# Optimization experiments

Measured on AMD Instinct MI355X. Metric: run time of the kernel, lower is better.

The kernel has to match this reference:

```python
import jax, jax.numpy as jnp
import numpy as np

N, L, D = 8192, 50, 64          # nodes, max history length, embed_dim
NUM_USERS = 100000
NUM_ITEMS = 100000
NUM_RATINGS = 5


def setup_inputs() -> dict:
    key = jax.random.key(0)
    ks = jax.random.split(key, 12)
    g = lambda k, shp, s=0.05: jax.random.normal(k, shp, jnp.float32) * s
    return {
        "nodes": jax.random.randint(ks[0], (N,), 0, NUM_USERS),
        "history_uv": jax.random.randint(ks[1], (N, L), 0, NUM_ITEMS),
        "history_r": jax.random.randint(ks[2], (N, L), 0, NUM_RATINGS),
        "hist_len": jax.random.randint(ks[3], (N,), 1, L + 1),  # ragged lengths in [1, L]
        # embedding tables (v2e / u2e / r2e)
        "v2e": g(ks[4], (NUM_ITEMS, D), 0.1),
        "u2e": g(ks[5], (NUM_USERS, D), 0.1),
        "r2e": g(ks[6], (NUM_RATINGS, D), 0.1),
        # w_r1: Dense(2D -> D), w_r2: Dense(D -> D)
        "W1": g(ks[7], (2 * D, D)), "b1": jnp.zeros((D,), jnp.float32),
        "W2": g(ks[8], (D, D)), "b2": jnp.zeros((D,), jnp.float32),
        # Attention MLP: Dense(2D->D), Dense(D->D), Dense(D->1)
        "A1": g(ks[9], (2 * D, D)), "ab1": jnp.zeros((D,), jnp.float32),
        "A2": g(ks[10], (D, D)), "ab2": jnp.zeros((D,), jnp.float32),
        "A3": g(ks[11], (D, 1)), "ab3": jnp.zeros((1,), jnp.float32),
    }


def reference(nodes, history_uv, history_r, hist_len, v2e, u2e, r2e,
              W1, b1, W2, b2, A1, ab1, A2, ab2, A3, ab3):
    # Vectorized form of the per-node Python loop: pad histories to L, mask.
    e_uv = v2e[history_uv]                       # [N,L,D] neighbor item embeds
    uv_rep = u2e[nodes]                          # [N,D]   self (user) embed
    e_r = r2e[history_r]                         # [N,L,D] rating embeds
    x = jnp.concatenate([e_uv, e_r], axis=-1)    # [N,L,2D]
    x = jax.nn.relu(x @ W1 + b1)                 # w_r1 + relu
    o = jax.nn.relu(x @ W2 + b2)                 # w_r2 + relu -> o_history [N,L,D]
    # attention: concat(o_history, repeated uv_rep) -> 2-layer relu MLP -> scalar
    a_in = jnp.concatenate(
        [o, jnp.broadcast_to(uv_rep[:, None, :], o.shape)], axis=-1)  # [N,L,2D]
    h = jax.nn.relu(a_in @ A1 + ab1)
    h = jax.nn.relu(h @ A2 + ab2)
    s = (h @ A3 + ab3)[..., 0]                   # [N,L] attention logits
    mask = jnp.arange(L)[None, :] < hist_len[:, None]
    att = jax.nn.softmax(jnp.where(mask, s, -1e9), axis=-1)  # softmax over history
    # att_history = o_history^T @ att_w, per node -> [N,D]
    return jnp.einsum('nl,nld->nd', att, o)
```

## Files before the change

### kernel.cpp

```cpp
#include <hip/hip_runtime.h>
#include <hip/hip_bf16.h>
#include <stdint.h>

typedef short bfx8 __attribute__((ext_vector_type(8)));
typedef float f32x4 __attribute__((ext_vector_type(4)));

#define MFMA16(a, b, c) __builtin_amdgcn_mfma_f32_16x16x32_bf16(a, b, c, 0, 0, 0)
#define STAGE_FENCE() __builtin_amdgcn_sched_barrier(0x77)
#define PIN_FENCE()   __builtin_amdgcn_sched_barrier(0x47)

#define OFF_W1 0
#define OFF_A1 8192
#define OFF_W2 24576
#define OFF_A2 32768
#define OFF_CB 40960
#define OFF_TB 42256
#define CBB_B1  0
#define CBB_B2  256
#define CBB_AB1 512
#define CBB_AB2 768
#define CBB_A3  1024

__device__ __forceinline__ uint32_t pk2(float a, float b) {
    __hip_bfloat162 h = __float22bfloat162_rn(make_float2(a, b));
    union { __hip_bfloat162 h; uint32_t u; } cv; cv.h = h; return cv.u;
}
__device__ __forceinline__ float bflo(uint32_t w) { return __uint_as_float(w << 16); }
__device__ __forceinline__ float bfhi(uint32_t w) { return __uint_as_float(w & 0xFFFF0000u); }

__device__ __forceinline__ bfx8 pack8(const float4 a, const float4 b) {
    union { bfx8 v; uint32_t u[4]; } r;
    r.u[0] = pk2(a.x, a.y); r.u[1] = pk2(a.z, a.w);
    r.u[2] = pk2(b.x, b.y); r.u[3] = pk2(b.z, b.w);
    return r.v;
}
__device__ __forceinline__ bfx8 packr(f32x4 a, f32x4 b) {
    union { bfx8 v; uint32_t u[4]; } r;
    r.u[0] = pk2(fmaxf(a[0], 0.f), fmaxf(a[1], 0.f));
    r.u[1] = pk2(fmaxf(a[2], 0.f), fmaxf(a[3], 0.f));
    r.u[2] = pk2(fmaxf(b[0], 0.f), fmaxf(b[1], 0.f));
    r.u[3] = pk2(fmaxf(b[2], 0.f), fmaxf(b[3], 0.f));
    return r.v;
}
__device__ __forceinline__ float4 ld4(const float* p) { return *(const float4*)p; }

__device__ __forceinline__ int mix4(int row) {
    return (row & 3) | (((row >> 4) & 1) << 2) | (((row >> 3) & 1) << 3);
}
__device__ __forceinline__ int mix3(int row) {
    return (row & 3) | (((row >> 3) & 1) << 2);
}
template <int CTRL>
__device__ __forceinline__ float dppadd(float x) {
    int y = __builtin_amdgcn_update_dpp(0, __float_as_int(x), CTRL, 0xF, 0xF, false);
    return x + __int_as_float(y);
}
__device__ __forceinline__ float rowsum16(float x) {
    x = dppadd<0xB1>(x);
    x = dppadd<0x4E>(x);
    x = dppadd<0x124>(x);
    x = dppadd<0x128>(x);
    return x;
}

__global__ __launch_bounds__(512, 1) void uvagg_mfma(
    const int* __restrict__ nodes, const int* __restrict__ huv,
    const int* __restrict__ hr, const int* __restrict__ hlen,
    const float* __restrict__ v2e, const float* __restrict__ u2e,
    const float* __restrict__ r2e,
    const float* __restrict__ W1, const float* __restrict__ b1,
    const float* __restrict__ W2, const float* __restrict__ b2,
    const float* __restrict__ A1, const float* __restrict__ ab1,
    const float* __restrict__ A2, const float* __restrict__ ab2,
    const float* __restrict__ A3, const float* __restrict__ ab3f,
    float* __restrict__ out, int N, int L, int nwaves)
{
    __shared__ __align__(16) uint8_t smem[43616];
    float* cbf = (float*)(smem + OFF_CB);

    const int tid = threadIdx.x;
    for (int i = tid; i < 4096; i += 512) {
        int kp = i >> 6, d = i & 63;
        int addr = d * 256 + ((((kp >> 2) ^ mix4(d)) & 15) << 4) + ((kp & 3) << 2);
        *(uint32_t*)(smem + OFF_A1 + addr) = pk2(A1[(2 * kp) * 64 + d], A1[(2 * kp + 1) * 64 + d]);
    }
    for (int i = tid; i < 2048; i += 512) {
        int kp = i >> 6, d = i & 63;
        int addr = d * 128 + ((((kp >> 2) ^ mix3(d)) & 7) << 4) + ((kp & 3) << 2);
        *(uint32_t*)(smem + OFF_W1 + addr) = pk2(W1[(2 * kp) * 64 + d], W1[(2 * kp + 1) * 64 + d]);
        *(uint32_t*)(smem + OFF_W2 + addr) = pk2(W2[(2 * kp) * 64 + d], W2[(2 * kp + 1) * 64 + d]);
        *(uint32_t*)(smem + OFF_A2 + addr) = pk2(A2[(2 * kp) * 64 + d], A2[(2 * kp + 1) * 64 + d]);
    }
    for (int i = tid; i < 321; i += 512) {
        if (i < 64)       cbf[i]   = b1[i];
        else if (i < 128) cbf[i]   = b2[i - 64];
        else if (i < 192) cbf[i]   = ab1[i - 128];
        else if (i < 256) cbf[i]   = ab2[i - 192];
        else if (i < 320) cbf[i]   = A3[i - 256];
        else              cbf[320] = ab3f[0];
    }
    for (int i = tid; i < 320; i += 512) {
        const int rr_ = i >> 6, d = i & 63;
        const float* wcol = W1 + 64 * 64 + d;
        const float* rrow = r2e + rr_ * 64;
        float a0 = b1[d], a1 = 0.f, a2 = 0.f, a3 = 0.f;
        #pragma unroll
        for (int k2 = 0; k2 < 64; k2 += 4) {
            a0 = fmaf(wcol[(k2 + 0) * 64], rrow[k2 + 0], a0);
            a1 = fmaf(wcol[(k2 + 1) * 64], rrow[k2 + 1], a1);
            a2 = fmaf(wcol[(k2 + 2) * 64], rrow[k2 + 2], a2);
            a3 = fmaf(wcol[(k2 + 3) * 64], rrow[k2 + 3], a3);
        }
        *(float*)(smem + OFF_TB + rr_ * 272 + d * 4) = (a0 + a1) + (a2 + a3);
    }
    __syncthreads();

    const int lane = tid & 63;
    const int wid  = tid >> 6;
    const int s    = lane & 15;
    const int g    = lane >> 4;
    const int r    = s & 3;
    const int q    = s >> 2;
    const int rs   = 8 * q + r;

    const int cx = ((q >> 1) | ((q & 1) << 1));
    const int base1 = rs * 256 + ((g ^ r) << 4) + (cx << 6);
    const int base2 = rs * 128 + ((g ^ r) << 4) + ((q & 1) << 6);
    const uint8_t* pw2 = smem + (base1 ^ (2 << 6));
    const uint8_t* pw3 = smem + (base1 ^ (3 << 6));
    const uint8_t* pa0 = smem + (base1 ^ (0 << 6));
    const uint8_t* pa1 = smem + (base1 ^ (1 << 6));
    const uint8_t* pq0 = smem + (base2 ^ (0 << 6));
    const uint8_t* pq1 = smem + (base2 ^ (1 << 6));
    const uint8_t* pcb = smem + OFF_CB + 32 * g;
    const uint8_t* ptb = smem + OFF_TB + 32 * g;
    const float ab3 = cbf[320];

    for (int node = blockIdx.x * 8 + wid; node < N; node += nwaves) {
        const int hl = __builtin_amdgcn_readfirstlane(min(hlen[node], L));
        const int un = __builtin_amdgcn_readfirstlane(nodes[node]);

        const float* ur = u2e + (size_t)un * 64;
        const bfx8 uf2 = pack8(ld4(ur + 8 * g),      ld4(ur + 8 * g + 4));
        const bfx8 uf3 = pack8(ld4(ur + 32 + 8 * g), ld4(ur + 36 + 8 * g));

        const int idxlane = min(lane, L - 1);
        const int iu_all = huv[(size_t)node * L + idxlane];
        const int ir_all = hr [(size_t)node * L + idxlane];

        f32x4 h1base[4];
        #pragma unroll
        for (int mt = 0; mt < 4; ++mt) {
            const int dof = 4 * (mt & 1) + 32 * (mt >> 1);
            h1base[mt] = *(const f32x4*)(pcb + CBB_AB1 + dof * 4);
            h1base[mt] = MFMA16(*(const bfx8*)(pw2 + OFF_A1 + dof * 256), uf2, h1base[mt]);
            h1base[mt] = MFMA16(*(const bfx8*)(pw3 + OFF_A1 + dof * 256), uf3, h1base[mt]);
        }

        float zacc = 0.0f;
        f32x4 accO[4];
        #pragma unroll
        for (int i = 0; i < 4; ++i) accO[i] = f32x4{0.f, 0.f, 0.f, 0.f};

        const int ntile = (hl + 15) >> 4;

        float4 qa0, qa1, qa2, qa3;
        int irs;
        {
            const int slot0 = min(s, hl - 1);
            const int iu = __shfl(iu_all, slot0, 64);
            irs = __shfl(ir_all, slot0, 64);
            const float* vr = v2e + (size_t)iu * 64;
            qa0 = ld4(vr + 8 * g);      qa1 = ld4(vr + 8 * g + 4);
            qa2 = ld4(vr + 32 + 8 * g); qa3 = ld4(vr + 36 + 8 * g);
        }

        for (int tt = 0; tt < ntile; ++tt) {
            const int gslot = tt * 16 + s;
            const bfx8 f0 = pack8(qa0, qa1);
            const bfx8 f1 = pack8(qa2, qa3);
            const uint8_t* ptbr = ptb + irs * 272;

            f32x4 ah[4];
            #pragma unroll
            for (int mt = 0; mt < 4; ++mt) {
                const int dof = 4 * (mt & 1) + 32 * (mt >> 1);
                ah[mt] = *(const f32x4*)(ptbr + dof * 4);
                ah[mt] = MFMA16(*(const bfx8*)(pq0 + OFF_W1 + dof * 128), f0, ah[mt]);
                ah[mt] = MFMA16(*(const bfx8*)(pq1 + OFF_W1 + dof * 128), f1, ah[mt]);
            }
            const bfx8 x1a = packr(ah[0], ah[1]);
            const bfx8 x1b = packr(ah[2], ah[3]);

            if (tt + 1 < ntile) {
                const int nslot = min(tt * 16 + 16 + s, hl - 1);
                const int niu = __shfl(iu_all, nslot, 64);
                irs = __shfl(ir_all, nslot, 64);
                const float* vr = v2e + (size_t)niu * 64;
                qa0 = ld4(vr + 8 * g);      qa1 = ld4(vr + 8 * g + 4);
                qa2 = ld4(vr + 32 + 8 * g); qa3 = ld4(vr + 36 + 8 * g);
            }
            PIN_FENCE();

            f32x4 ao[4];
            #pragma unroll
            for (int mt = 0; mt < 4; ++mt) {
                const int dof = 4 * (mt & 1) + 32 * (mt >> 1);
                ao[mt] = *(const f32x4*)(pcb + CBB_B2 + dof * 4);
                ao[mt] = MFMA16(*(const bfx8*)(pq0 + OFF_W2 + dof * 128), x1a, ao[mt]);
                ao[mt] = MFMA16(*(const bfx8*)(pq1 + OFF_W2 + dof * 128), x1b, ao[mt]);
            }
            const bfx8 oa = packr(ao[0], ao[1]);
            const bfx8 ob = packr(ao[2], ao[3]);
            STAGE_FENCE();

            f32x4 h[4];
            #pragma unroll
            for (int mt = 0; mt < 4; ++mt) {
                const int dof = 4 * (mt & 1) + 32 * (mt >> 1);
                h[mt] = h1base[mt];
                h[mt] = MFMA16(*(const bfx8*)(pa0 + OFF_A1 + dof * 256), oa, h[mt]);
                h[mt] = MFMA16(*(const bfx8*)(pa1 + OFF_A1 + dof * 256), ob, h[mt]);
            }
            const bfx8 h1a = packr(h[0], h[1]);
            const bfx8 h1b = packr(h[2], h[3]);
            STAGE_FENCE();

            float part = 0.0f;
            #pragma unroll
            for (int mt = 0; mt < 4; ++mt) {
                const int dof = 4 * (mt & 1) + 32 * (mt >> 1);
                f32x4 h2 = *(const f32x4*)(pcb + CBB_AB2 + dof * 4);
                h2 = MFMA16(*(const bfx8*)(pq0 + OFF_A2 + dof * 128), h1a, h2);
                h2 = MFMA16(*(const bfx8*)(pq1 + OFF_A2 + dof * 128), h1b, h2);
                const f32x4 aq = *(const f32x4*)(pcb + CBB_A3 + dof * 4);
                part = fmaf(fmaxf(h2[0], 0.f), aq[0], part);
                part = fmaf(fmaxf(h2[1], 0.f), aq[1], part);
                part = fmaf(fmaxf(h2[2], 0.f), aq[2], part);
                part = fmaf(fmaxf(h2[3], 0.f), aq[3], part);
            }
            STAGE_FENCE();
            float p2 = part + __shfl_xor(part, 16, 64);
            const float sl = p2 + __shfl_xor(p2, 32, 64) + ab3;
            const float p = (gslot < hl) ? __expf(sl) : 0.0f;
            zacc += p;
            union { bfx8 v; uint32_t u[4]; } ua, ub;
            ua.v = oa; ub.v = ob;
            #pragma unroll
            for (int j = 0; j < 2; ++j) {
                accO[0][2*j+0] = fmaf(p, bflo(ua.u[j]),     accO[0][2*j+0]);
                accO[0][2*j+1] = fmaf(p, bfhi(ua.u[j]),     accO[0][2*j+1]);
                accO[1][2*j+0] = fmaf(p, bflo(ua.u[2 + j]), accO[1][2*j+0]);
                accO[1][2*j+1] = fmaf(p, bfhi(ua.u[2 + j]), accO[1][2*j+1]);
                accO[2][2*j+0] = fmaf(p, bflo(ub.u[j]),     accO[2][2*j+0]);
                accO[2][2*j+1] = fmaf(p, bfhi(ub.u[j]),     accO[2][2*j+1]);
                accO[3][2*j+0] = fmaf(p, bflo(ub.u[2 + j]), accO[3][2*j+0]);
                accO[3][2*j+1] = fmaf(p, bfhi(ub.u[2 + j]), accO[3][2*j+1]);
            }
        }

        const float Z = rowsum16(zacc);
        #pragma unroll
        for (int mt = 0; mt < 4; ++mt)
            #pragma unroll
            for (int rr2 = 0; rr2 < 4; ++rr2)
                accO[mt][rr2] = rowsum16(accO[mt][rr2]);
        const float inv = 1.0f / Z;
        if (s == 0) {
            float* op = out + (size_t)node * 64;
            #pragma unroll
            for (int mt = 0; mt < 4; ++mt) {
                const int dof = 8 * g + 4 * (mt & 1) + 32 * (mt >> 1);
                *(float4*)(op + dof) = make_float4(accO[mt][0] * inv, accO[mt][1] * inv,
                                                   accO[mt][2] * inv, accO[mt][3] * inv);
            }
        }
    }
}

extern "C" void kernel_launch(void* const* d_in, const int* in_sizes, int n_in,
                              void* d_out, int out_size, void* d_ws, size_t ws_size,
                              hipStream_t stream) {
    const int*   nodes = (const int*)d_in[0];
    const int*   huv   = (const int*)d_in[1];
    const int*   hrr   = (const int*)d_in[2];
    const int*   hlen  = (const int*)d_in[3];
    const float* v2e   = (const float*)d_in[4];
    const float* u2e   = (const float*)d_in[5];
    const float* r2e   = (const float*)d_in[6];
    const float* W1    = (const float*)d_in[7];
    const float* b1    = (const float*)d_in[8];
    const float* W2    = (const float*)d_in[9];
    const float* b2    = (const float*)d_in[10];
    const float* A1    = (const float*)d_in[11];
    const float* ab1   = (const float*)d_in[12];
    const float* A2    = (const float*)d_in[13];
    const float* ab2   = (const float*)d_in[14];
    const float* A3    = (const float*)d_in[15];
    const float* ab3   = (const float*)d_in[16];
    float* out = (float*)d_out;

    const int N = in_sizes[0];
    const int L = in_sizes[1] / N;

    int blocks = (N + 7) / 8;
    if (blocks > 768) blocks = 768;
    const int nwaves = blocks * 8;

    hipLaunchKernelGGL(uvagg_mfma, dim3(blocks), dim3(512), 0, stream,
                       nodes, huv, hrr, hlen, v2e, u2e, r2e,
                       W1, b1, W2, b2, A1, ab1, A2, ab2, A3, ab3,
                       out, N, L, nwaves);
}
```

Measured before the change: 41.51 us.

## Sort nodes by history-length bin and pair long/short nodes per wave

Adds three small pre-kernels that bucket nodes by tile count (ceil(hist_len/16)), prefix-scan the per-wave bin counts, and scatter node indices into a sorted permutation. The main kernel then gives each wave a pair of nodes taken from opposite ends of the sorted order, so every wave gets a roughly equal amount of work. The grid is also reduced to 512 blocks. This targets the tail imbalance caused by ragged history lengths, at the cost of three extra kernel launches and an indirect node lookup.

New measurement: 47.34 us. +14.0%, slower.

```diff
diff --git a/kernel.cpp b/kernel.cpp
--- a/kernel.cpp
+++ b/kernel.cpp
@@ -63,6 +63,54 @@
     return x;
 }
 
+__global__ __launch_bounds__(256) void bin_count(const int* __restrict__ hlen,
+                                                 int N, int L, int* __restrict__ wavecnt) {
+    const int i = blockIdx.x * 256 + threadIdx.x;
+    const int ww = i >> 6, lane = i & 63;
+    const int NW = (N + 63) >> 6;
+    int bin = -1;
+    if (i < N) bin = ((min(hlen[i], L) + 15) >> 4) - 1;
+    #pragma unroll
+    for (int b = 0; b < 4; ++b) {
+        unsigned long long m = __ballot(bin == b);
+        if (lane == 0 && ww < NW) wavecnt[b * NW + ww] = __popcll(m);
+    }
+}
+
+__global__ __launch_bounds__(512) void bin_scan(int* __restrict__ wavecnt, int n) {
+    __shared__ int sa[512], sb[512];
+    const int t = threadIdx.x;
+    const int v = (t < n) ? wavecnt[t] : 0;
+    sa[t] = v;
+    __syncthreads();
+    int* src = sa; int* dst = sb;
+    #pragma unroll
+    for (int off = 1; off < 512; off <<= 1) {
+        dst[t] = src[t] + ((t >= off) ? src[t - off] : 0);
+        __syncthreads();
+        int* tmp = src; src = dst; dst = tmp;
+    }
+    if (t < n) wavecnt[t] = src[t] - v;
+}
+
+__global__ __launch_bounds__(256) void bin_scatter(const int* __restrict__ hlen,
+                                                   int N, int L,
+                                                   const int* __restrict__ offs,
+                                                   int* __restrict__ perm) {
+    const int i = blockIdx.x * 256 + threadIdx.x;
+    const int ww = i >> 6, lane = i & 63;
+    const int NW = (N + 63) >> 6;
+    const int bin = (i < N) ? (((min(hlen[i], L) + 15) >> 4) - 1) : -1;
+    #pragma unroll
+    for (int b = 0; b < 4; ++b) {
+        unsigned long long m = __ballot(bin == b);
+        if (bin == b) {
+            int rank = __popcll(m & ((1ULL << lane) - 1ULL));
+            perm[offs[b * NW + ww] + rank] = i;
+        }
+    }
+}
+
 __global__ __launch_bounds__(512, 1) void uvagg_mfma(
     const int* __restrict__ nodes, const int* __restrict__ huv,
     const int* __restrict__ hr, const int* __restrict__ hlen,
@@ -73,7 +121,8 @@
     const float* __restrict__ A1, const float* __restrict__ ab1,
     const float* __restrict__ A2, const float* __restrict__ ab2,
     const float* __restrict__ A3, const float* __restrict__ ab3f,
-    float* __restrict__ out, int N, int L, int nwaves)
+    float* __restrict__ out, int N, int L, int nwaves,
+    const int* __restrict__ perm)
 {
     __shared__ __align__(16) uint8_t smem[43616];
     float* cbf = (float*)(smem + OFF_CB);
@@ -136,143 +185,157 @@
     const uint8_t* ptb = smem + OFF_TB + 32 * g;
     const float ab3 = cbf[320];
 
-    for (int node = blockIdx.x * 8 + wid; node < N; node += nwaves) {
-        const int hl = __builtin_amdgcn_readfirstlane(min(hlen[node], L));
-        const int un = __builtin_amdgcn_readfirstlane(nodes[node]);
-
-        const float* ur = u2e + (size_t)un * 64;
-        const bfx8 uf2 = pack8(ld4(ur + 8 * g),      ld4(ur + 8 * g + 4));
-        const bfx8 uf3 = pack8(ld4(ur + 32 + 8 * g), ld4(ur + 36 + 8 * g));
-
-        const int idxlane = min(lane, L - 1);
-        const int iu_all = huv[(size_t)node * L + idxlane];
-        const int ir_all = hr [(size_t)node * L + idxlane];
-
-        f32x4 h1base[4];
-        #pragma unroll
-        for (int mt = 0; mt < 4; ++mt) {
-            const int dof = 4 * (mt & 1) + 32 * (mt >> 1);
-            h1base[mt] = *(const f32x4*)(pcb + CBB_AB1 + dof * 4);
-            h1base[mt] = MFMA16(*(const bfx8*)(pw2 + OFF_A1 + dof * 256), uf2, h1base[mt]);
-            h1base[mt] = MFMA16(*(const bfx8*)(pw3 + OFF_A1 + dof * 256), uf3, h1base[mt]);
-        }
-
-        float zacc = 0.0f;
-        f32x4 accO[4];
-        #pragma unroll
-        for (int i = 0; i < 4; ++i) accO[i] = f32x4{0.f, 0.f, 0.f, 0.f};
-
-        const int ntile = (hl + 15) >> 4;
-
-        float4 qa0, qa1, qa2, qa3;
-        int irs;
-        {
-            const int slot0 = min(s, hl - 1);
-            const int iu = __shfl(iu_all, slot0, 64);
-            irs = __shfl(ir_all, slot0, 64);
-            const float* vr = v2e + (size_t)iu * 64;
-            qa0 = ld4(vr + 8 * g);      qa1 = ld4(vr + 8 * g + 4);
-            qa2 = ld4(vr + 32 + 8 * g); qa3 = ld4(vr + 36 + 8 * g);
-        }
-
-        for (int tt = 0; tt < ntile; ++tt) {
-            const int gslot = tt * 16 + s;
-            const bfx8 f0 = pack8(qa0, qa1);
-            const bfx8 f1 = pack8(qa2, qa3);
-            const uint8_t* ptbr = ptb + irs * 272;
-
-            f32x4 ah[4];
+    const int w = blockIdx.x * 8 + wid;
+    const int half = (N + 1) >> 1;
+
+    for (int k = w; k < half; k += nwaves) {
+        const int k2v = N - 1 - k;
+        #pragma unroll 1
+        for (int j = 0; j < 2; ++j) {
+            int node;
+            if (j == 0) node = __builtin_amdgcn_readfirstlane(perm[k]);
+            else {
+                if (k2v < half) break;
+                node = __builtin_amdgcn_readfirstlane(perm[k2v]);
+            }
+
+            const int hl = __builtin_amdgcn_readfirstlane(min(hlen[node], L));
+            const int un = __builtin_amdgcn_readfirstlane(nodes[node]);
+
+            const float* ur = u2e + (size_t)un * 64;
+            const bfx8 uf2 = pack8(ld4(ur + 8 * g),      ld4(ur + 8 * g + 4));
+            const bfx8 uf3 = pack8(ld4(ur + 32 + 8 * g), ld4(ur + 36 + 8 * g));
+
+            const int idxlane = min(lane, L - 1);
+            const int iu_all = huv[(size_t)node * L + idxlane];
+            const int ir_all = hr [(size_t)node * L + idxlane];
+
+            f32x4 h1base[4];
             #pragma unroll
             for (int mt = 0; mt < 4; ++mt) {
                 const int dof = 4 * (mt & 1) + 32 * (mt >> 1);
-                ah[mt] = *(const f32x4*)(ptbr + dof * 4);
-                ah[mt] = MFMA16(*(const bfx8*)(pq0 + OFF_W1 + dof * 128), f0, ah[mt]);
-                ah[mt] = MFMA16(*(const bfx8*)(pq1 + OFF_W1 + dof * 128), f1, ah[mt]);
-            }
-            const bfx8 x1a = packr(ah[0], ah[1]);
-            const bfx8 x1b = packr(ah[2], ah[3]);
-
-            if (tt + 1 < ntile) {
-                const int nslot = min(tt * 16 + 16 + s, hl - 1);
-                const int niu = __shfl(iu_all, nslot, 64);
-                irs = __shfl(ir_all, nslot, 64);
-                const float* vr = v2e + (size_t)niu * 64;
+                h1base[mt] = *(const f32x4*)(pcb + CBB_AB1 + dof * 4);
+                h1base[mt] = MFMA16(*(const bfx8*)(pw2 + OFF_A1 + dof * 256), uf2, h1base[mt]);
+                h1base[mt] = MFMA16(*(const bfx8*)(pw3 + OFF_A1 + dof * 256), uf3, h1base[mt]);
+            }
+
+            float zacc = 0.0f;
+            f32x4 accO[4];
+            #pragma unroll
+            for (int i = 0; i < 4; ++i) accO[i] = f32x4{0.f, 0.f, 0.f, 0.f};
+
+            const int ntile = (hl + 15) >> 4;
+
+            float4 qa0, qa1, qa2, qa3;
+            int irs;
+            {
+                const int slot0 = min(s, hl - 1);
+                const int iu = __shfl(iu_all, slot0, 64);
+                irs = __shfl(ir_all, slot0, 64);
+                const float* vr = v2e + (size_t)iu * 64;
                 qa0 = ld4(vr + 8 * g);      qa1 = ld4(vr + 8 * g + 4);
                 qa2 = ld4(vr + 32 + 8 * g); qa3 = ld4(vr + 36 + 8 * g);
             }
-            PIN_FENCE();
-
-            f32x4 ao[4];
+
+            for (int tt = 0; tt < ntile; ++tt) {
+                const int gslot = tt * 16 + s;
+                const bfx8 f0 = pack8(qa0, qa1);
+                const bfx8 f1 = pack8(qa2, qa3);
+                const uint8_t* ptbr = ptb + irs * 272;
+
+                f32x4 ah[4];
+                #pragma unroll
+                for (int mt = 0; mt < 4; ++mt) {
+                    const int dof = 4 * (mt & 1) + 32 * (mt >> 1);
+                    ah[mt] = *(const f32x4*)(ptbr + dof * 4);
+                    ah[mt] = MFMA16(*(const bfx8*)(pq0 + OFF_W1 + dof * 128), f0, ah[mt]);
+                    ah[mt] = MFMA16(*(const bfx8*)(pq1 + OFF_W1 + dof * 128), f1, ah[mt]);
+                }
+                const bfx8 x1a = packr(ah[0], ah[1]);
+                const bfx8 x1b = packr(ah[2], ah[3]);
+
+                if (tt + 1 < ntile) {
+                    const int nslot = min(tt * 16 + 16 + s, hl - 1);
+                    const int niu = __shfl(iu_all, nslot, 64);
+                    irs = __shfl(ir_all, nslot, 64);
+                    const float* vr = v2e + (size_t)niu * 64;
+                    qa0 = ld4(vr + 8 * g);      qa1 = ld4(vr + 8 * g + 4);
+                    qa2 = ld4(vr + 32 + 8 * g); qa3 = ld4(vr + 36 + 8 * g);
+                }
+                PIN_FENCE();
+
+                f32x4 ao[4];
+                #pragma unroll
+                for (int mt = 0; mt < 4; ++mt) {
+                    const int dof = 4 * (mt & 1) + 32 * (mt >> 1);
+                    ao[mt] = *(const f32x4*)(pcb + CBB_B2 + dof * 4);
+                    ao[mt] = MFMA16(*(const bfx8*)(pq0 + OFF_W2 + dof * 128), x1a, ao[mt]);
+                    ao[mt] = MFMA16(*(const bfx8*)(pq1 + OFF_W2 + dof * 128), x1b, ao[mt]);
+                }
+                const bfx8 oa = packr(ao[0], ao[1]);
+                const bfx8 ob = packr(ao[2], ao[3]);
+                STAGE_FENCE();
+
+                f32x4 h[4];
+                #pragma unroll
+                for (int mt = 0; mt < 4; ++mt) {
+                    const int dof = 4 * (mt & 1) + 32 * (mt >> 1);
+                    h[mt] = h1base[mt];
+                    h[mt] = MFMA16(*(const bfx8*)(pa0 + OFF_A1 + dof * 256), oa, h[mt]);
+                    h[mt] = MFMA16(*(const bfx8*)(pa1 + OFF_A1 + dof * 256), ob, h[mt]);
+                }
+                const bfx8 h1a = packr(h[0], h[1]);
+                const bfx8 h1b = packr(h[2], h[3]);
+                STAGE_FENCE();
+
+                float part = 0.0f;
+                #pragma unroll
+                for (int mt = 0; mt < 4; ++mt) {
+                    const int dof = 4 * (mt & 1) + 32 * (mt >> 1);
+                    f32x4 h2 = *(const f32x4*)(pcb + CBB_AB2 + dof * 4);
+                    h2 = MFMA16(*(const bfx8*)(pq0 + OFF_A2 + dof * 128), h1a, h2);
+                    h2 = MFMA16(*(const bfx8*)(pq1 + OFF_A2 + dof * 128), h1b, h2);
+                    const f32x4 aq = *(const f32x4*)(pcb + CBB_A3 + dof * 4);
+                    part = fmaf(fmaxf(h2[0], 0.f), aq[0], part);
+                    part = fmaf(fmaxf(h2[1], 0.f), aq[1], part);
+                    part = fmaf(fmaxf(h2[2], 0.f), aq[2], part);
+                    part = fmaf(fmaxf(h2[3], 0.f), aq[3], part);
+                }
+                STAGE_FENCE();
+                float p2 = part + __shfl_xor(part, 16, 64);
+                const float sl = p2 + __shfl_xor(p2, 32, 64) + ab3;
+                const float p = (gslot < hl) ? __expf(sl) : 0.0f;
+                zacc += p;
+                union { bfx8 v; uint32_t u[4]; } ua, ub;
+                ua.v = oa; ub.v = ob;
+                #pragma unroll
+                for (int jj = 0; jj < 2; ++jj) {
+                    accO[0][2*jj+0] = fmaf(p, bflo(ua.u[jj]),     accO[0][2*jj+0]);
+                    accO[0][2*jj+1] = fmaf(p, bfhi(ua.u[jj]),     accO[0][2*jj+1]);
+                    accO[1][2*jj+0] = fmaf(p, bflo(ua.u[2 + jj]), accO[1][2*jj+0]);
+                    accO[1][2*jj+1] = fmaf(p, bfhi(ua.u[2 + jj]), accO[1][2*jj+1]);
+                    accO[2][2*jj+0] = fmaf(p, bflo(ub.u[jj]),     accO[2][2*jj+0]);
+                    accO[2][2*jj+1] = fmaf(p, bfhi(ub.u[jj]),     accO[2][2*jj+1]);
+                    accO[3][2*jj+0] = fmaf(p, bflo(ub.u[2 + jj]), accO[3][2*jj+0]);
+                    accO[3][2*jj+1] = fmaf(p, bfhi(ub.u[2 + jj]), accO[3][2*jj+1]);
+                }
+            }
+
+            const float Z = rowsum16(zacc);
             #pragma unroll
-            for (int mt = 0; mt < 4; ++mt) {
-                const int dof = 4 * (mt & 1) + 32 * (mt >> 1);
-                ao[mt] = *(const f32x4*)(pcb + CBB_B2 + dof * 4);
-                ao[mt] = MFMA16(*(const bfx8*)(pq0 + OFF_W2 + dof * 128), x1a, ao[mt]);
-                ao[mt] = MFMA16(*(const bfx8*)(pq1 + OFF_W2 + dof * 128), x1b, ao[mt]);
-            }
-            const bfx8 oa = packr(ao[0], ao[1]);
-            const bfx8 ob = packr(ao[2], ao[3]);
-            STAGE_FENCE();
-
-            f32x4 h[4];
-            #pragma unroll
-            for (int mt = 0; mt < 4; ++mt) {
-                const int dof = 4 * (mt & 1) + 32 * (mt >> 1);
-                h[mt] = h1base[mt];
-                h[mt] = MFMA16(*(const bfx8*)(pa0 + OFF_A1 + dof * 256), oa, h[mt]);
-                h[mt] = MFMA16(*(const bfx8*)(pa1 + OFF_A1 + dof * 256), ob, h[mt]);
-            }
-            const bfx8 h1a = packr(h[0], h[1]);
-            const bfx8 h1b = packr(h[2], h[3]);
-            STAGE_FENCE();
-
-            float part = 0.0f;
-            #pragma unroll
-            for (int mt = 0; mt < 4; ++mt) {
-                const int dof = 4 * (mt & 1) + 32 * (mt >> 1);
-                f32x4 h2 = *(const f32x4*)(pcb + CBB_AB2 + dof * 4);
-                h2 = MFMA16(*(const bfx8*)(pq0 + OFF_A2 + dof * 128), h1a, h2);
-                h2 = MFMA16(*(const bfx8*)(pq1 + OFF_A2 + dof * 128), h1b, h2);
-                const f32x4 aq = *(const f32x4*)(pcb + CBB_A3 + dof * 4);
-                part = fmaf(fmaxf(h2[0], 0.f), aq[0], part);
-                part = fmaf(fmaxf(h2[1], 0.f), aq[1], part);
-                part = fmaf(fmaxf(h2[2], 0.f), aq[2], part);
-                part = fmaf(fmaxf(h2[3], 0.f), aq[3], part);
-            }
-            STAGE_FENCE();
-            float p2 = part + __shfl_xor(part, 16, 64);
-            const float sl = p2 + __shfl_xor(p2, 32, 64) + ab3;
-            const float p = (gslot < hl) ? __expf(sl) : 0.0f;
-            zacc += p;
-            union { bfx8 v; uint32_t u[4]; } ua, ub;
-            ua.v = oa; ub.v = ob;
-            #pragma unroll
-            for (int j = 0; j < 2; ++j) {
-                accO[0][2*j+0] = fmaf(p, bflo(ua.u[j]),     accO[0][2*j+0]);
-                accO[0][2*j+1] = fmaf(p, bfhi(ua.u[j]),     accO[0][2*j+1]);
-                accO[1][2*j+0] = fmaf(p, bflo(ua.u[2 + j]), accO[1][2*j+0]);
-                accO[1][2*j+1] = fmaf(p, bfhi(ua.u[2 + j]), accO[1][2*j+1]);
-                accO[2][2*j+0] = fmaf(p, bflo(ub.u[j]),     accO[2][2*j+0]);
-                accO[2][2*j+1] = fmaf(p, bfhi(ub.u[j]),     accO[2][2*j+1]);
-                accO[3][2*j+0] = fmaf(p, bflo(ub.u[2 + j]), accO[3][2*j+0]);
-                accO[3][2*j+1] = fmaf(p, bfhi(ub.u[2 + j]), accO[3][2*j+1]);
-            }
-        }
-
-        const float Z = rowsum16(zacc);
-        #pragma unroll
-        for (int mt = 0; mt < 4; ++mt)
-            #pragma unroll
-            for (int rr2 = 0; rr2 < 4; ++rr2)
-                accO[mt][rr2] = rowsum16(accO[mt][rr2]);
-        const float inv = 1.0f / Z;
-        if (s == 0) {
-            float* op = out + (size_t)node * 64;
-            #pragma unroll
-            for (int mt = 0; mt < 4; ++mt) {
-                const int dof = 8 * g + 4 * (mt & 1) + 32 * (mt >> 1);
-                *(float4*)(op + dof) = make_float4(accO[mt][0] * inv, accO[mt][1] * inv,
-                                                   accO[mt][2] * inv, accO[mt][3] * inv);
+            for (int mt = 0; mt < 4; ++mt)
+                #pragma unroll
+                for (int rr2 = 0; rr2 < 4; ++rr2)
+                    accO[mt][rr2] = rowsum16(accO[mt][rr2]);
+            const float inv = 1.0f / Z;
+            if (s == 0) {
+                float* op = out + (size_t)node * 64;
+                #pragma unroll
+                for (int mt = 0; mt < 4; ++mt) {
+                    const int dof = 8 * g + 4 * (mt & 1) + 32 * (mt >> 1);
+                    *(float4*)(op + dof) = make_float4(accO[mt][0] * inv, accO[mt][1] * inv,
+                                                       accO[mt][2] * inv, accO[mt][3] * inv);
+                }
             }
         }
     }
@@ -302,13 +365,22 @@
 
     const int N = in_sizes[0];
     const int L = in_sizes[1] / N;
-
-    int blocks = (N + 7) / 8;
-    if (blocks > 768) blocks = 768;
+    const int NW = (N + 63) >> 6;
+
+    int* wavecnt = (int*)d_ws;
+    int* perm    = (int*)((uint8_t*)d_ws + 2048);
+
+    hipLaunchKernelGGL(bin_count, dim3((N + 255) / 256), dim3(256), 0, stream,
+                       hlen, N, L, wavecnt);
+    hipLaunchKernelGGL(bin_scan, dim3(1), dim3(512), 0, stream, wavecnt, 4 * NW);
+    hipLaunchKernelGGL(bin_scatter, dim3((N + 255) / 256), dim3(256), 0, stream,
+                       hlen, N, L, wavecnt, perm);
+
+    int blocks = (N + 15) / 16;
+    if (blocks > 512) blocks = 512;
     const int nwaves = blocks * 8;
-
     hipLaunchKernelGGL(uvagg_mfma, dim3(blocks), dim3(512), 0, stream,
                        nodes, huv, hrr, hlen, v2e, u2e, r2e,
                        W1, b1, W2, b2, A1, ab1, A2, ab2, A3, ab3,
-                       out, N, L, nwaves);
-}
+                       out, N, L, nwaves, perm);
+}
```
